# Kernel tuning notes

Measured on AMD Instinct MI355X. Metric: run time of the kernel, lower is better.

Reference implementation:

```python
import jax, jax.numpy as jnp
import numpy as np

B, L, H, DI, N, R, K = 1, 1024, 2048, 4096, 16, 128, 4


def setup_inputs() -> dict:
    key = jax.random.key(0)
    ks = jax.random.split(key, 12)
    s = 0.02
    x = jax.random.normal(ks[0], (B, L, H), jnp.float32)
    W_in_states = jax.random.normal(ks[1], (DI, H), jnp.float32) * s
    W_in_gates = jax.random.normal(ks[2], (DI, H), jnp.float32) * s
    conv_w = jax.random.normal(ks[3], (DI, K), jnp.float32) * 0.2
    conv_b = jax.random.normal(ks[4], (DI,), jnp.float32) * 0.02
    W_dt = jax.random.normal(ks[5], (R, DI), jnp.float32) * s
    W_b = jax.random.normal(ks[6], (N, DI), jnp.float32) * s
    W_c = jax.random.normal(ks[7], (N, DI), jnp.float32) * s
    W_dtproj = jax.random.normal(ks[8], (DI, R), jnp.float32) * 0.1
    # dt bias so softplus(dt) is in a realistic small range
    b_dtproj = jax.random.uniform(ks[9], (DI,), jnp.float32, minval=-5.0, maxval=-3.0)
    A_log = jnp.log(jnp.broadcast_to(jnp.arange(1, N + 1, dtype=jnp.float32), (DI, N)))
    D = jnp.ones((DI,), jnp.float32)
    W_out = jax.random.normal(ks[10], (H, DI), jnp.float32) * s
    return {"x": x, "W_in_states": W_in_states, "W_in_gates": W_in_gates,
            "conv_w": conv_w, "conv_b": conv_b, "W_dt": W_dt, "W_b": W_b,
            "W_c": W_c, "W_dtproj": W_dtproj, "b_dtproj": b_dtproj,
            "A_log": A_log, "D": D, "W_out": W_out}


def _silu(v):
    return v * jax.nn.sigmoid(v)


def reference(x, W_in_states, W_in_gates, conv_w, conv_b, W_dt, W_b, W_c,
              W_dtproj, b_dtproj, A_log, D, W_out):
    b, l, _ = x.shape
    # input projections -> [B, DI, L]
    hs = jnp.einsum('blh,dh->bdl', x, W_in_states)
    gate = jnp.einsum('blh,dh->bdl', x, W_in_gates)
    # causal depthwise conv1d (kernel K, left pad K-1, truncate to L)
    k = conv_w.shape[-1]
    xpad = jnp.pad(hs, ((0, 0), (0, 0), (k - 1, 0)))
    conv = sum(conv_w[None, :, j, None] * xpad[:, :, j:j + l] for j in range(k))
    conv = conv + conv_b[None, :, None]
    hs = _silu(conv)                       # [B, DI, L]
    hst = hs.transpose(0, 2, 1)            # [B, L, DI]
    # data-dependent SSM params
    time_step = jnp.einsum('bld,rd->blr', hst, W_dt)           # [B, L, R]
    dt = jax.nn.softplus(time_step @ W_dtproj.T + b_dtproj)    # [B, L, DI]
    Bm = jnp.einsum('bld,nd->bln', hst, W_b)                   # [B, L, N]
    Cm = jnp.einsum('bld,nd->bln', hst, W_c)                   # [B, L, N]
    A = -jnp.exp(A_log)                                        # [DI, N]
    dt_bdl = dt.transpose(0, 2, 1)                             # [B, DI, L]
    dA = jnp.exp(A[None, :, None, :] * dt_bdl[:, :, :, None])  # [B, DI, L, N]
    dBu = dt_bdl[:, :, :, None] * Bm[:, None, :, :] * hs[:, :, :, None]
    # sequential selective scan over L
    dA_l = dA.transpose(2, 0, 1, 3)    # [L, B, DI, N]
    dBu_l = dBu.transpose(2, 0, 1, 3)

    def step(s, inp):
        a, bu = inp
        s = a * s + bu
        return s, s

    init = jnp.zeros((b, hs.shape[1], A_log.shape[1]), hs.dtype)
    _, h = jax.lax.scan(step, init, (dA_l, dBu_l))   # [L, B, DI, N]
    y = jnp.einsum('lbdn,bln->bdl', h, Cm)           # contract state dim
    y = y + hs * D[None, :, None]
    y = y * _silu(gate)
    out = jnp.einsum('bdl,od->blo', y, W_out)        # [B, L, H]
    return out
```

## Files before the change

### kernel.cpp

```cpp
#include <hip/hip_runtime.h>

#define SEQ 1024
#define HID 2048
#define DIN 4096
#define NST 16
#define RNK 128
#define CHN 64
#define CLEN 16

typedef __attribute__((ext_vector_type(4))) float f32x4;
typedef __attribute__((ext_vector_type(4))) __bf16 bf16x4v;
typedef __attribute__((ext_vector_type(8))) __bf16 bf16x8v;
typedef __attribute__((ext_vector_type(8))) unsigned short u16x8;

#define GPTR(p) ((const __attribute__((address_space(1))) void*)(p))
#define LPTR(p) ((__attribute__((address_space(3))) void*)(p))

__device__ __forceinline__ unsigned short f2bf(float v) {
  unsigned u = __builtin_bit_cast(unsigned, v);
  u = (u + 0x7fffu + ((u >> 16) & 1u)) >> 16;
  return (unsigned short)u;
}
__device__ __forceinline__ float softplus_f(float x) {
  return (x > 20.f) ? x : log1pf(__expf(x));
}
__device__ __forceinline__ float silu_f(float x) {
  return x / (1.f + __expf(-x));
}

#define CV_NX  (SEQ*HID)
#define CV_NW  (DIN*HID)
#define CV_NDT (RNK*DIN)
#define CV_NB  (NST*DIN)
#define CV_NPD (32*DIN)
#define CV_NWO (HID*DIN)
#define CV_TOT (CV_NX + 2*CV_NW + CV_NDT + 2*CV_NB + CV_NPD + CV_NDT + CV_NWO)

__global__ __launch_bounds__(256) void cvt_all(
    const float* __restrict__ x, const float* __restrict__ wis,
    const float* __restrict__ wig, const float* __restrict__ wdt,
    const float* __restrict__ wb, const float* __restrict__ wc,
    const float* __restrict__ wdtp, const float* __restrict__ wout,
    unsigned short* __restrict__ x_bf, unsigned short* __restrict__ wis_bf,
    unsigned short* __restrict__ wig_bf, unsigned short* __restrict__ wcat_bf,
    unsigned short* __restrict__ wdtp_bf, unsigned short* __restrict__ wout_bf)
{
  size_t j = ((size_t)blockIdx.x * 256 + threadIdx.x) * 8;
  const float* src = nullptr; unsigned short* dst;
  if (j < CV_NX) { src = x + j; dst = x_bf + j; }
  else if ((j -= CV_NX) < CV_NW) { src = wis + j; dst = wis_bf + j; }
  else if ((j -= CV_NW) < CV_NW) { src = wig + j; dst = wig_bf + j; }
  else if ((j -= CV_NW) < CV_NDT) { src = wdt + j; dst = wcat_bf + j; }
  else if ((j -= CV_NDT) < CV_NB) { src = wb + j; dst = wcat_bf + (size_t)128*DIN + j; }
  else if ((j -= CV_NB) < CV_NB) { src = wc + j; dst = wcat_bf + (size_t)144*DIN + j; }
  else if ((j -= CV_NB) < CV_NPD) { dst = wcat_bf + (size_t)160*DIN + j; }
  else if ((j -= CV_NPD) < CV_NDT) { src = wdtp + j; dst = wdtp_bf + j; }
  else { j -= CV_NDT; src = wout + j; dst = wout_bf + j; }
  u16x8 o = {};
  if (src) {
    f32x4 a = *(const f32x4*)src;
    f32x4 b = *(const f32x4*)(src + 4);
#pragma unroll
    for (int i = 0; i < 4; i++) { o[i] = f2bf(a[i]); o[4 + i] = f2bf(b[i]); }
  }
  *(u16x8*)dst = o;
}

template<int EPI>
__global__ __launch_bounds__(256) void gemm128(
    const unsigned short* __restrict__ Ag, const unsigned short* __restrict__ Bg,
    float* __restrict__ Cg, const float* __restrict__ bias,
    int Msz, int Nsz, int Kstride, int Kiter)
{
  __shared__ __align__(16) unsigned short As[3][128 * 32];
  __shared__ __align__(16) unsigned short Bs[3][128 * 32];
  const int kz = blockIdx.z;
  Ag += (size_t)kz * Kiter;
  Bg += (size_t)kz * Kiter;
  Cg += (size_t)kz * Msz * Nsz;
  const int nwg = gridDim.x * gridDim.y;
  const int orig = blockIdx.y * gridDim.x + blockIdx.x;
  const int swz = (orig & 7) * (nwg >> 3) + (orig >> 3);
  const int bx = swz % gridDim.x, by = swz / gridDim.x;
  const int tid = threadIdx.x;
  const int m0 = bx * 128, n0 = by * 128;
  const int lane = tid & 63, w = tid >> 6;
  const int wm = w >> 1, wn = w & 1;
  const int lg = lane >> 4, lr = lane & 15;
  const int srow = w * 32 + (lane >> 2);
  const int sch = (((lane & 3) ^ ((lane >> 3) & 3))) * 8;
  const unsigned short* Ag0 = Ag + (size_t)(m0 + srow) * Kstride + sch;
  const unsigned short* Bg0 = Bg + (size_t)(n0 + srow) * Kstride + sch;
  const int wo = w * 1024;
  const int lgs = (lg ^ ((lr >> 1) & 3)) * 8;

  auto stage = [&](int b, int k0) {
    __builtin_amdgcn_global_load_lds(GPTR(Ag0 + k0), LPTR(&As[b][wo]), 16, 0, 0);
    __builtin_amdgcn_global_load_lds(GPTR(Ag0 + 16 * Kstride + k0), LPTR(&As[b][wo + 512]), 16, 0, 0);
    __builtin_amdgcn_global_load_lds(GPTR(Bg0 + k0), LPTR(&Bs[b][wo]), 16, 0, 0);
    __builtin_amdgcn_global_load_lds(GPTR(Bg0 + 16 * Kstride + k0), LPTR(&Bs[b][wo + 512]), 16, 0, 0);
  };

  const int nt = Kiter >> 5;
  stage(0, 0);
  stage(1, 32);
  f32x4 acc[4][4] = {};
  int cur = 0, pf = 2;
  for (int t = 0; t < nt; ++t) {
    if (t < nt - 1) {
      asm volatile("s_waitcnt vmcnt(4)" ::: "memory");
    } else {
      asm volatile("s_waitcnt vmcnt(0)" ::: "memory");
    }
    __builtin_amdgcn_s_barrier();
    asm volatile("" ::: "memory");
    if (t + 2 < nt) stage(pf, (t + 2) * 32);
    bf16x8v af[4], bfv[4];
#pragma unroll
    for (int mi = 0; mi < 4; mi++)
      af[mi] = *(const bf16x8v*)&As[cur][(wm * 64 + mi * 16 + lr) * 32 + lgs];
#pragma unroll
    for (int ni = 0; ni < 4; ni++)
      bfv[ni] = *(const bf16x8v*)&Bs[cur][(wn * 64 + ni * 16 + lr) * 32 + lgs];
#pragma unroll
    for (int mi = 0; mi < 4; mi++)
#pragma unroll
      for (int ni = 0; ni < 4; ni++)
        acc[mi][ni] = __builtin_amdgcn_mfma_f32_16x16x32_bf16(af[mi], bfv[ni], acc[mi][ni], 0, 0, 0);
    cur = (cur == 2) ? 0 : cur + 1;
    pf = (pf == 2) ? 0 : pf + 1;
  }
#pragma unroll
  for (int mi = 0; mi < 4; mi++) {
#pragma unroll
    for (int ni = 0; ni < 4; ni++) {
      const int col = n0 + wn * 64 + ni * 16 + lr;
#pragma unroll
      for (int r = 0; r < 4; r++) {
        const int row = m0 + wm * 64 + mi * 16 + lg * 4 + r;
        float v = acc[mi][ni][r];
        if (EPI == 1) v = softplus_f(v + bias[col]);
        Cg[(size_t)row * Nsz + col] = v;
      }
    }
  }
}

template<int EPI>
__global__ __launch_bounds__(256) void gemm_nt(
    const unsigned short* __restrict__ Ag, const unsigned short* __restrict__ Bg,
    float* __restrict__ Cg, const float* __restrict__ bias,
    int Msz, int Nsz, int Kstride, int Kiter)
{
  __shared__ __align__(16) unsigned short As[128][40];
  __shared__ __align__(16) unsigned short Bs[64][40];
  const int kz = blockIdx.z;
  Ag += (size_t)kz * Kiter;
  Bg += (size_t)kz * Kiter;
  Cg += (size_t)kz * Msz * Nsz;
  const int tid = threadIdx.x;
  const int m0 = blockIdx.x * 128, n0 = blockIdx.y * 64;
  const int lane = tid & 63, w = tid >> 6;
  const int wm = w >> 1, wn = w & 1;
  const int lg = lane >> 4, lr = lane & 15;
  const int r4 = tid >> 2, c8 = (tid & 3) * 8;
  f32x4 acc[4][2] = {};
  for (int k0 = 0; k0 < Kiter; k0 += 32) {
    uint4 a0 = *(const uint4*)(Ag + (size_t)(m0 + r4) * Kstride + k0 + c8);
    uint4 a1 = *(const uint4*)(Ag + (size_t)(m0 + 64 + r4) * Kstride + k0 + c8);
    uint4 b0 = *(const uint4*)(Bg + (size_t)(n0 + r4) * Kstride + k0 + c8);
    *(uint4*)&As[r4][c8] = a0;
    *(uint4*)&As[64 + r4][c8] = a1;
    *(uint4*)&Bs[r4][c8] = b0;
    __syncthreads();
    bf16x8v af[4], bfr[2];
#pragma unroll
    for (int mi = 0; mi < 4; mi++) {
      const int row = wm * 64 + mi * 16 + lr;
      bf16x4v lo = *(const bf16x4v*)&As[row][4 * lg];
      bf16x4v hi = *(const bf16x4v*)&As[row][16 + 4 * lg];
      af[mi] = __builtin_shufflevector(lo, hi, 0, 1, 2, 3, 4, 5, 6, 7);
    }
#pragma unroll
    for (int ni = 0; ni < 2; ni++) {
      const int row = wn * 32 + ni * 16 + lr;
      bf16x4v lo = *(const bf16x4v*)&Bs[row][4 * lg];
      bf16x4v hi = *(const bf16x4v*)&Bs[row][16 + 4 * lg];
      bfr[ni] = __builtin_shufflevector(lo, hi, 0, 1, 2, 3, 4, 5, 6, 7);
    }
#pragma unroll
    for (int mi = 0; mi < 4; mi++)
#pragma unroll
      for (int ni = 0; ni < 2; ni++)
        acc[mi][ni] = __builtin_amdgcn_mfma_f32_16x16x32_bf16(af[mi], bfr[ni], acc[mi][ni], 0, 0, 0);
    __syncthreads();
  }
#pragma unroll
  for (int mi = 0; mi < 4; mi++) {
#pragma unroll
    for (int ni = 0; ni < 2; ni++) {
      const int col = n0 + wn * 32 + ni * 16 + lr;
#pragma unroll
      for (int r = 0; r < 4; r++) {
        const int row = m0 + wm * 64 + mi * 16 + lg * 4 + r;
        float v = acc[mi][ni][r];
        if (EPI == 1) v = softplus_f(v + bias[col]);
        Cg[(size_t)row * Nsz + col] = v;
      }
    }
  }
}

__global__ __launch_bounds__(256) void conv_silu(
    const float* __restrict__ pg, const float* __restrict__ cw,
    const float* __restrict__ cb, float* __restrict__ hs,
    unsigned short* __restrict__ hs_bf)
{
  int idx = blockIdx.x * 256 + threadIdx.x;
  int l = idx >> 12, d = idx & (DIN - 1);
  float acc = cb[d];
#pragma unroll
  for (int j = 0; j < 4; j++) {
    int ll = l + j - 3;
    float v = (ll >= 0) ? pg[(size_t)ll * 8192 + d] : 0.f;
    acc = fmaf(cw[d * 4 + j], v, acc);
  }
  float r = silu_f(acc);
  hs[idx] = r;
  hs_bf[idx] = f2bf(r);
}

__global__ __launch_bounds__(256) void reduce_ts(
    const float* __restrict__ c2p, float* __restrict__ c2,
    unsigned short* __restrict__ ts_bf)
{
  int i = blockIdx.x * 256 + threadIdx.x;
  float s = 0.f;
#pragma unroll
  for (int z = 0; z < 8; z++) s += c2p[(size_t)z * SEQ * 192 + i];
  c2[i] = s;
  int l = i / 192, col = i - l * 192;
  if (col < 128) ts_bf[l * 128 + col] = f2bf(s);
}

__global__ __launch_bounds__(256) void reduce_out(
    const float* __restrict__ p, float* __restrict__ out)
{
  int i = (blockIdx.x * 256 + threadIdx.x) * 4;
  float4 a = *(const float4*)&p[i];
#pragma unroll
  for (int z = 1; z < 4; z++) {
    float4 b = *(const float4*)&p[(size_t)z * SEQ * HID + i];
    a.x += b.x; a.y += b.y; a.z += b.z; a.w += b.w;
  }
  *(float4*)&out[i] = a;
}

__global__ __launch_bounds__(256) void scan_phase1(
    const float* __restrict__ dt, const float* __restrict__ hs,
    const float* __restrict__ c2, const float* __restrict__ alog,
    float* __restrict__ Pbuf, float* __restrict__ Sbuf)
{
  __shared__ float B_ch[CLEN][16];
  const int tid = threadIdx.x;
  const int d = blockIdx.x * 256 + tid;
  const int c = blockIdx.y;
  const int l0 = c * CLEN;
  B_ch[tid >> 4][tid & 15] = c2[(size_t)(l0 + (tid >> 4)) * 192 + 128 + (tid & 15)];
  float a[16];
#pragma unroll
  for (int i = 0; i < 16; i++) a[i] = -__expf(alog[(size_t)d * 16 + i]);
  __syncthreads();
  float s[16] = {};
  float P[16];
#pragma unroll
  for (int i = 0; i < 16; i++) P[i] = 1.f;
  for (int t = 0; t < CLEN; t++) {
    float dtv = dt[(size_t)(l0 + t) * DIN + d];
    float u = hs[(size_t)(l0 + t) * DIN + d];
    float w = dtv * u;
#pragma unroll
    for (int n = 0; n < 16; n++) {
      float dA = __expf(a[n] * dtv);
      s[n] = fmaf(dA, s[n], w * B_ch[t][n]);
      P[n] *= dA;
    }
  }
  size_t base = ((size_t)c * DIN + d) * 16;
#pragma unroll
  for (int i = 0; i < 4; i++) {
    *(float4*)&Sbuf[base + 4 * i] = *(float4*)&s[4 * i];
    *(float4*)&Pbuf[base + 4 * i] = *(float4*)&P[4 * i];
  }
}

__global__ __launch_bounds__(256) void scan_phase2(
    const float* __restrict__ Pbuf, float* __restrict__ Sbuf)
{
  size_t idx = (size_t)blockIdx.x * 256 + threadIdx.x;
  const size_t stride = (size_t)DIN * 16;
  float s = 0.f;
#pragma unroll 4
  for (int c = 0; c < CHN; c++) {
    float Pv = Pbuf[c * stride + idx];
    float Sv = Sbuf[c * stride + idx];
    Sbuf[c * stride + idx] = s;
    s = fmaf(Pv, s, Sv);
  }
}

__global__ __launch_bounds__(256) void scan_phase3(
    const float* __restrict__ dt, const float* __restrict__ hs,
    const float* __restrict__ pg, const float* __restrict__ c2,
    const float* __restrict__ alog, const float* __restrict__ Dv,
    const float* __restrict__ sig, unsigned short* __restrict__ ygT)
{
  __shared__ float B_ch[CLEN][16], C_ch[CLEN][16];
  const int tid = threadIdx.x;
  const int d = blockIdx.x * 256 + tid;
  const int c = blockIdx.y;
  const int l0 = c * CLEN;
  {
    int t = tid >> 4, n = tid & 15;
    B_ch[t][n] = c2[(size_t)(l0 + t) * 192 + 128 + n];
    C_ch[t][n] = c2[(size_t)(l0 + t) * 192 + 144 + n];
  }
  float a[16];
#pragma unroll
  for (int i = 0; i < 16; i++) a[i] = -__expf(alog[(size_t)d * 16 + i]);
  const float Dd = Dv[d];
  float s[16];
  size_t base = ((size_t)c * DIN + d) * 16;
#pragma unroll
  for (int i = 0; i < 4; i++) *(float4*)&s[4 * i] = *(const float4*)&sig[base + 4 * i];
  __syncthreads();
  for (int t = 0; t < CLEN; t++) {
    float dtv = dt[(size_t)(l0 + t) * DIN + d];
    float u = hs[(size_t)(l0 + t) * DIN + d];
    float g = pg[(size_t)(l0 + t) * 8192 + 4096 + d];
    float w = dtv * u;
    float y = 0.f;
#pragma unroll
    for (int n = 0; n < 16; n++) {
      float dA = __expf(a[n] * dtv);
      s[n] = fmaf(dA, s[n], w * B_ch[t][n]);
      y = fmaf(s[n], C_ch[t][n], y);
    }
    float o = (y + u * Dd) * silu_f(g);
    ygT[(size_t)(l0 + t) * DIN + d] = f2bf(o);
  }
}

extern "C" void kernel_launch(void* const* d_in, const int* in_sizes, int n_in,
                              void* d_out, int out_size, void* d_ws, size_t ws_size,
                              hipStream_t stream) {
  const float* x     = (const float*)d_in[0];
  const float* wis   = (const float*)d_in[1];
  const float* wig   = (const float*)d_in[2];
  const float* convw = (const float*)d_in[3];
  const float* convb = (const float*)d_in[4];
  const float* wdt   = (const float*)d_in[5];
  const float* wb    = (const float*)d_in[6];
  const float* wc    = (const float*)d_in[7];
  const float* wdtp  = (const float*)d_in[8];
  const float* bdtp  = (const float*)d_in[9];
  const float* alog  = (const float*)d_in[10];
  const float* Dv    = (const float*)d_in[11];
  const float* wout  = (const float*)d_in[12];

  char* ws = (char*)d_ws;
  size_t off = 0;
  auto alloc = [&](size_t bytes) { void* p = ws + off; off += (bytes + 255) & ~(size_t)255; return p; };
  unsigned short* x_bf    = (unsigned short*)alloc((size_t)SEQ * HID * 2);
  unsigned short* wis_bf  = (unsigned short*)alloc((size_t)DIN * HID * 2);
  unsigned short* wig_bf  = (unsigned short*)alloc((size_t)DIN * HID * 2);
  unsigned short* wcat_bf = (unsigned short*)alloc((size_t)192 * DIN * 2);
  unsigned short* wdtp_bf = (unsigned short*)alloc((size_t)DIN * RNK * 2);
  unsigned short* wout_bf = (unsigned short*)alloc((size_t)HID * DIN * 2);
  float* pg    = (float*)alloc((size_t)SEQ * 8192 * 4);
  float* hs2   = (float*)alloc((size_t)SEQ * DIN * 4);
  unsigned short* hs_bf = (unsigned short*)alloc((size_t)SEQ * DIN * 2);
  float* c2    = (float*)alloc((size_t)SEQ * 192 * 4);
  float* c2p   = (float*)alloc((size_t)8 * SEQ * 192 * 4);
  unsigned short* ts_bf = (unsigned short*)alloc((size_t)SEQ * RNK * 2);
  float* dtbuf = (float*)alloc((size_t)SEQ * DIN * 4);
  unsigned short* ygT_bf = (unsigned short*)alloc((size_t)SEQ * DIN * 2);
  if (off > ws_size) return;
  float* Pbuf = (float*)wis_bf;
  float* Sbuf = (float*)wig_bf;
  float* op_part = pg;

  cvt_all<<<CV_TOT / 2048, 256, 0, stream>>>(x, wis, wig, wdt, wb, wc, wdtp, wout,
                                             x_bf, wis_bf, wig_bf, wcat_bf, wdtp_bf, wout_bf);
  gemm128<0><<<dim3(SEQ / 128, 8192 / 128), 256, 0, stream>>>(x_bf, wis_bf, pg, nullptr, SEQ, 8192, HID, HID);
  conv_silu<<<(SEQ * DIN) / 256, 256, 0, stream>>>(pg, convw, convb, hs2, hs_bf);
  gemm_nt<0><<<dim3(SEQ / 128, 192 / 64, 8), 256, 0, stream>>>(hs_bf, wcat_bf, c2p, nullptr, SEQ, 192, DIN, DIN / 8);
  reduce_ts<<<(SEQ * 192) / 256, 256, 0, stream>>>(c2p, c2, ts_bf);
  gemm_nt<1><<<dim3(SEQ / 128, DIN / 64), 256, 0, stream>>>(ts_bf, wdtp_bf, dtbuf, bdtp, SEQ, DIN, RNK, RNK);
  scan_phase1<<<dim3(DIN / 256, CHN), 256, 0, stream>>>(dtbuf, hs2, c2, alog, Pbuf, Sbuf);
  scan_phase2<<<(DIN * NST) / 256, 256, 0, stream>>>(Pbuf, Sbuf);
  scan_phase3<<<dim3(DIN / 256, CHN), 256, 0, stream>>>(dtbuf, hs2, pg, c2, alog, Dv, Sbuf, ygT_bf);
  gemm128<0><<<dim3(SEQ / 128, HID / 128, 4), 256, 0, stream>>>(ygT_bf, wout_bf, op_part, nullptr, SEQ, HID, DIN, DIN / 4);
  reduce_out<<<(SEQ * HID) / 1024, 256, 0, stream>>>(op_part, (float*)d_out);
}
```

Before: 226.8 us.

## Double K-tile depth to 64 with double-buffered LDS and new XOR swizzle

Raises the GEMM K-step from 32 to 64 and replaces the three-stage 32-wide LDS ring with a two-stage 64-wide buffer. The LDS swizzle and global-to-LDS load mapping are reworked to an 8-slot XOR pattern, and each iteration issues two MFMA sweeps. This halves the number of barriers and loop iterations per tile. In exchange the pipeline is shallower (one tile in flight, full vmcnt(0) wait each step), and LDS use grows from 48KB to 64KB, which may reduce occupancy.

```diff
diff --git a/kernel.cpp b/kernel.cpp
--- a/kernel.cpp
+++ b/kernel.cpp
@@ -72,8 +72,8 @@
     float* __restrict__ Cg, const float* __restrict__ bias,
     int Msz, int Nsz, int Kstride, int Kiter)
 {
-  __shared__ __align__(16) unsigned short As[3][128 * 32];
-  __shared__ __align__(16) unsigned short Bs[3][128 * 32];
+  __shared__ __align__(16) unsigned short As[2][128 * 64];
+  __shared__ __align__(16) unsigned short Bs[2][128 * 64];
   const int kz = blockIdx.z;
   Ag += (size_t)kz * Kiter;
   Bg += (size_t)kz * Kiter;
@@ -87,48 +87,57 @@
   const int lane = tid & 63, w = tid >> 6;
   const int wm = w >> 1, wn = w & 1;
   const int lg = lane >> 4, lr = lane & 15;
-  const int srow = w * 32 + (lane >> 2);
-  const int sch = (((lane & 3) ^ ((lane >> 3) & 3))) * 8;
-  const unsigned short* Ag0 = Ag + (size_t)(m0 + srow) * Kstride + sch;
-  const unsigned short* Bg0 = Bg + (size_t)(n0 + srow) * Kstride + sch;
-  const int wo = w * 1024;
-  const int lgs = (lg ^ ((lr >> 1) & 3)) * 8;
+  const int srow = w * 32 + (lane >> 3);
+  const int sslot = (lane & 7) ^ (lane >> 3);
+  const unsigned short* Ag0 = Ag + (size_t)(m0 + srow) * Kstride + sslot * 8;
+  const unsigned short* Bg0 = Bg + (size_t)(n0 + srow) * Kstride + sslot * 8;
+  const int ldso = w * 2048;
 
   auto stage = [&](int b, int k0) {
-    __builtin_amdgcn_global_load_lds(GPTR(Ag0 + k0), LPTR(&As[b][wo]), 16, 0, 0);
-    __builtin_amdgcn_global_load_lds(GPTR(Ag0 + 16 * Kstride + k0), LPTR(&As[b][wo + 512]), 16, 0, 0);
-    __builtin_amdgcn_global_load_lds(GPTR(Bg0 + k0), LPTR(&Bs[b][wo]), 16, 0, 0);
-    __builtin_amdgcn_global_load_lds(GPTR(Bg0 + 16 * Kstride + k0), LPTR(&Bs[b][wo + 512]), 16, 0, 0);
+#pragma unroll
+    for (int i = 0; i < 4; i++)
+      __builtin_amdgcn_global_load_lds(GPTR(Ag0 + (size_t)(i * 8) * Kstride + k0),
+                                       LPTR(&As[b][ldso + i * 512]), 16, 0, 0);
+#pragma unroll
+    for (int i = 0; i < 4; i++)
+      __builtin_amdgcn_global_load_lds(GPTR(Bg0 + (size_t)(i * 8) * Kstride + k0),
+                                       LPTR(&Bs[b][ldso + i * 512]), 16, 0, 0);
   };
 
-  const int nt = Kiter >> 5;
+  const int nt = Kiter >> 6;
   stage(0, 0);
-  stage(1, 32);
   f32x4 acc[4][4] = {};
-  int cur = 0, pf = 2;
+  int cur = 0;
+  const int rsw = lr & 7;
   for (int t = 0; t < nt; ++t) {
-    if (t < nt - 1) {
-      asm volatile("s_waitcnt vmcnt(4)" ::: "memory");
-    } else {
-      asm volatile("s_waitcnt vmcnt(0)" ::: "memory");
-    }
+    asm volatile("s_waitcnt vmcnt(0)" ::: "memory");
     __builtin_amdgcn_s_barrier();
     asm volatile("" ::: "memory");
-    if (t + 2 < nt) stage(pf, (t + 2) * 32);
-    bf16x8v af[4], bfv[4];
+    if (t + 1 < nt) stage(cur ^ 1, (t + 1) * 64);
+    bf16x8v af0[4], bf0[4], af1[4], bf1[4];
+#pragma unroll
+    for (int mi = 0; mi < 4; mi++) {
+      const int row = (wm * 64 + mi * 16 + lr) * 64;
+      af0[mi] = *(const bf16x8v*)&As[cur][row + ((0 * 4 + lg) ^ rsw) * 8];
+      af1[mi] = *(const bf16x8v*)&As[cur][row + ((1 * 4 + lg) ^ rsw) * 8];
+    }
+#pragma unroll
+    for (int ni = 0; ni < 4; ni++) {
+      const int row = (wn * 64 + ni * 16 + lr) * 64;
+      bf0[ni] = *(const bf16x8v*)&Bs[cur][row + ((0 * 4 + lg) ^ rsw) * 8];
+      bf1[ni] = *(const bf16x8v*)&Bs[cur][row + ((1 * 4 + lg) ^ rsw) * 8];
+    }
 #pragma unroll
     for (int mi = 0; mi < 4; mi++)
-      af[mi] = *(const bf16x8v*)&As[cur][(wm * 64 + mi * 16 + lr) * 32 + lgs];
-#pragma unroll
-    for (int ni = 0; ni < 4; ni++)
-      bfv[ni] = *(const bf16x8v*)&Bs[cur][(wn * 64 + ni * 16 + lr) * 32 + lgs];
+#pragma unroll
+      for (int ni = 0; ni < 4; ni++)
+        acc[mi][ni] = __builtin_amdgcn_mfma_f32_16x16x32_bf16(af0[mi], bf0[ni], acc[mi][ni], 0, 0, 0);
 #pragma unroll
     for (int mi = 0; mi < 4; mi++)
 #pragma unroll
       for (int ni = 0; ni < 4; ni++)
-        acc[mi][ni] = __builtin_amdgcn_mfma_f32_16x16x32_bf16(af[mi], bfv[ni], acc[mi][ni], 0, 0, 0);
-    cur = (cur == 2) ? 0 : cur + 1;
-    pf = (pf == 2) ? 0 : pf + 1;
+        acc[mi][ni] = __builtin_amdgcn_mfma_f32_16x16x32_bf16(af1[mi], bf1[ni], acc[mi][ni], 0, 0, 0);
+    cur ^= 1;
   }
 #pragma unroll
   for (int mi = 0; mi < 4; mi++) {
```

Measured after the change: 215.5 us. -5.0%, faster.
